# Optimization experiments

Hardware: AMD Instinct MI355X
Metric: run time of the kernel (lower is better)

## Reference

```python
import jax, jax.numpy as jnp
import numpy as np

NUM_HEADS = 2  # embed_dim=8 fixed by n_wires=8 in QLayer

def setup_inputs() -> dict:
    key = jax.random.key(0)
    k1, k2, k3 = jax.random.split(key, 3)
    x = jax.random.normal(k1, (32, 2048, 8), dtype=jnp.float32)
    theta = jax.random.normal(k2, (8,), dtype=jnp.float32)       # trainable RX angles
    W_out = jax.random.normal(k3, (8, 8), dtype=jnp.float32) * 0.35  # out_proj weight (no bias)
    return {"x": x, "theta": theta, "W_out": W_out}

def reference(x, theta, W_out):
    B, S, E = x.shape
    H = NUM_HEADS
    d_k = E // H
    # Quantum layer: RX(x_i) then RX(theta_i) on wire i from |0>, measure PauliZ
    # => <Z_i> = cos(x_i + theta_i). k = q = v = this (three identical calls on x).
    h = jnp.cos(x + theta)                                  # [B, S, E]
    h = h.reshape(B, S, H, d_k).transpose(0, 2, 1, 3)        # [B, H, S, d_k]
    scale = 1.0 / jnp.sqrt(jnp.asarray(d_k, dtype=h.dtype))
    scores = jnp.einsum('bhqd,bhkd->bhqk', h, h) * scale     # [B, H, S, S]
    attn = jax.nn.softmax(scores, axis=-1)                   # dropout: eval-mode identity
    out = jnp.einsum('bhqk,bhkd->bhqd', attn, h)             # [B, H, S, d_k]
    out = out.transpose(0, 2, 1, 3).reshape(B, S, E)         # merge heads
    return out @ W_out.T                                     # nn.Linear(E, E, bias=False)
```

## Files before the change

### kernel.cpp

```cpp
#include <hip/hip_runtime.h>

#define NB 32
#define NS 2048
#define QS 0.72134752044448170367f

typedef _Float16 f16;
typedef _Float16 h2 __attribute__((ext_vector_type(2)));
typedef _Float16 h4 __attribute__((ext_vector_type(4)));
typedef _Float16 h8 __attribute__((ext_vector_type(8)));
typedef float f32x4 __attribute__((ext_vector_type(4)));

__device__ __forceinline__ h2 cvt_pk_f16(float a, float b) {
  return __builtin_bit_cast(h2, __builtin_amdgcn_cvt_pkrtz(a, b));
}
__device__ __forceinline__ f32x4 mfma16(h4 a, h4 b, f32x4 c) {
  return __builtin_amdgcn_mfma_f32_16x16x16f16(a, b, c, 0, 0, 0);
}

#define TR_STRIDE 1032
#define TR_BASE 8192
#define LDS_HALVES (8192 + 10 * 1032)
#define ZIDX (TR_BASE + 9 * TR_STRIDE)

__global__ __launch_bounds__(512, 4) void attn_fused_kernel(
    const float* __restrict__ x, const float* __restrict__ theta,
    const float* __restrict__ Wout, float* __restrict__ outp) {
  __shared__ __align__(16) f16 lds[LDS_HALVES];

  const int b = blockIdx.y;
  const int t = threadIdx.x;
  const int w = t >> 6;
  const int lane = t & 63;
  const int g = lane >> 4;
  const int n = lane & 15;

  float th[8];
#pragma unroll
  for (int e = 0; e < 8; ++e) th[e] = theta[e];

#pragma unroll
  for (int i = 0; i < 2; ++i) {
    const int l = t + 512 * i;
    const float4* xr = (const float4*)(x + ((size_t)b * NS + l) * 8);
    float4 lo = xr[0], hi = xr[1];
    h8 hv;
    hv[0] = (f16)__cosf(lo.x + th[0]);
    hv[1] = (f16)__cosf(lo.y + th[1]);
    hv[2] = (f16)__cosf(lo.z + th[2]);
    hv[3] = (f16)__cosf(lo.w + th[3]);
    hv[4] = (f16)__cosf(hi.x + th[4]);
    hv[5] = (f16)__cosf(hi.y + th[5]);
    hv[6] = (f16)__cosf(hi.z + th[6]);
    hv[7] = (f16)__cosf(hi.w + th[7]);
    ((h8*)lds)[l] = hv;
#pragma unroll
    for (int e = 0; e < 8; ++e) lds[TR_BASE + e * TR_STRIDE + l] = hv[e];
    lds[TR_BASE + 8 * TR_STRIDE + l] = (f16)1.0f;
    lds[ZIDX + l] = (f16)0.0f;
  }

  float4 pf[2][2];
#pragma unroll
  for (int i = 0; i < 2; ++i) {
    const int l = t + 512 * i;
    const float4* xr = (const float4*)(x + ((size_t)b * NS + 1024 + l) * 8);
    pf[i][0] = xr[0];
    pf[i][1] = xr[1];
  }

  h4 Bq0 = {(f16)0.f, (f16)0.f, (f16)0.f, (f16)0.f};
  h4 Bq1 = Bq0;
  if (g == 0) {
    const float4* xq = (const float4*)(
        x + ((size_t)b * NS + blockIdx.x * 128 + w * 16 + n) * 8);
    float4 lo = xq[0], hi = xq[1];
    Bq0[0] = (f16)(__cosf(lo.x + th[0]) * QS);
    Bq0[1] = (f16)(__cosf(lo.y + th[1]) * QS);
    Bq0[2] = (f16)(__cosf(lo.z + th[2]) * QS);
    Bq0[3] = (f16)(__cosf(lo.w + th[3]) * QS);
    Bq1[0] = (f16)(__cosf(hi.x + th[4]) * QS);
    Bq1[1] = (f16)(__cosf(hi.y + th[5]) * QS);
    Bq1[2] = (f16)(__cosf(hi.z + th[6]) * QS);
    Bq1[3] = (f16)(__cosf(hi.w + th[7]) * QS);
  }

  const int sini = (g == 0) ? n * 8 : ZIDX;
  const int sadv = (g == 0) ? 128 : 0;

  const int d0 = (n < 4) ? n : ((n == 4) ? 8 : 9);
  const int d1 = (n < 4) ? (n + 4) : d0;
  const int t0ini = TR_BASE + d0 * TR_STRIDE + 4 * g;
  const int t1ini = TR_BASE + d1 * TR_STRIDE + 4 * g;

  const f32x4 Z = {0.f, 0.f, 0.f, 0.f};
  f32x4 C0 = Z;
  f32x4 C1 = Z;

  __syncthreads();

  for (int chunk = 0; chunk < 2; ++chunk) {
    if (chunk == 1) {
      __syncthreads();
#pragma unroll
      for (int i = 0; i < 2; ++i) {
        const int l = t + 512 * i;
        float4 lo = pf[i][0], hi = pf[i][1];
        h8 hv;
        hv[0] = (f16)__cosf(lo.x + th[0]);
        hv[1] = (f16)__cosf(lo.y + th[1]);
        hv[2] = (f16)__cosf(lo.z + th[2]);
        hv[3] = (f16)__cosf(lo.w + th[3]);
        hv[4] = (f16)__cosf(hi.x + th[4]);
        hv[5] = (f16)__cosf(hi.y + th[5]);
        hv[6] = (f16)__cosf(hi.z + th[6]);
        hv[7] = (f16)__cosf(hi.w + th[7]);
        ((h8*)lds)[l] = hv;
#pragma unroll
        for (int e = 0; e < 8; ++e) lds[TR_BASE + e * TR_STRIDE + l] = hv[e];
      }
      __syncthreads();
    }

    int sa = sini;
    int ta0 = t0ini;
    int ta1 = t1ini;
#pragma unroll 4
    for (int kk = 0; kk < 64; ++kk) {
      h8 kr = *(const h8*)(lds + sa);
      h4 a0 = __builtin_shufflevector(kr, kr, 0, 1, 2, 3);
      h4 a1 = __builtin_shufflevector(kr, kr, 4, 5, 6, 7);
      h4 v0 = *(const h4*)(lds + ta0);
      h4 v1 = *(const h4*)(lds + ta1);

      f32x4 S0 = mfma16(a0, Bq0, Z);
      f32x4 S1 = mfma16(a1, Bq1, Z);

      h4 p0, p1;
      h2 u;
      u = cvt_pk_f16(__builtin_amdgcn_exp2f(S0[0]),
                     __builtin_amdgcn_exp2f(S0[1]));
      p0[0] = u[0];
      p0[1] = u[1];
      u = cvt_pk_f16(__builtin_amdgcn_exp2f(S0[2]),
                     __builtin_amdgcn_exp2f(S0[3]));
      p0[2] = u[0];
      p0[3] = u[1];
      u = cvt_pk_f16(__builtin_amdgcn_exp2f(S1[0]),
                     __builtin_amdgcn_exp2f(S1[1]));
      p1[0] = u[0];
      p1[1] = u[1];
      u = cvt_pk_f16(__builtin_amdgcn_exp2f(S1[2]),
                     __builtin_amdgcn_exp2f(S1[3]));
      p1[2] = u[0];
      p1[3] = u[1];

      C0 = mfma16(v0, p0, C0);
      C1 = mfma16(v1, p1, C1);

      sa += sadv;
      ta0 += 16;
      ta1 += 16;
    }
  }

  const float den0 = __shfl(C0[0], 16 + n, 64);
  const float den1 = __shfl(C1[0], 16 + n, 64);
  if (lane < 16) {
    const float i0 = 1.0f / den0, i1 = 1.0f / den1;
    float m8[8] = {C0[0] * i0, C0[1] * i0, C0[2] * i0, C0[3] * i0,
                   C1[0] * i1, C1[1] * i1, C1[2] * i1, C1[3] * i1};
    float o[8];
#pragma unroll
    for (int e = 0; e < 8; ++e) {
      float s = 0.f;
#pragma unroll
      for (int f = 0; f < 8; ++f) s += m8[f] * Wout[e * 8 + f];
      o[e] = s;
    }
    const int q = blockIdx.x * 128 + w * 16 + n;
    float4* op = (float4*)(outp + ((size_t)b * NS + q) * 8);
    op[0] = make_float4(o[0], o[1], o[2], o[3]);
    op[1] = make_float4(o[4], o[5], o[6], o[7]);
  }
}

extern "C" void kernel_launch(void* const* d_in, const int* in_sizes, int n_in,
                              void* d_out, int out_size, void* d_ws,
                              size_t ws_size, hipStream_t stream) {
  const float* x = (const float*)d_in[0];
  const float* theta = (const float*)d_in[1];
  const float* W = (const float*)d_in[2];
  float* out = (float*)d_out;
  (void)d_ws;
  (void)ws_size;

  attn_fused_kernel<<<dim3(NS / 128, NB), 512, 0, stream>>>(x, theta, W, out);
}
```

Baseline: 89.21 us.

## Split key range across two wave halves per query tile with LDS reduction

```diff
diff --git a/kernel.cpp b/kernel.cpp
--- a/kernel.cpp
+++ b/kernel.cpp
@@ -22,7 +22,7 @@
 #define LDS_HALVES (8192 + 10 * 1032)
 #define ZIDX (TR_BASE + 9 * TR_STRIDE)
 
-__global__ __launch_bounds__(512, 4) void attn_fused_kernel(
+__global__ __launch_bounds__(512, 8) void attn_fused_kernel(
     const float* __restrict__ x, const float* __restrict__ theta,
     const float* __restrict__ Wout, float* __restrict__ outp) {
   __shared__ __align__(16) f16 lds[LDS_HALVES];
@@ -33,6 +33,8 @@
   const int lane = t & 63;
   const int g = lane >> 4;
   const int n = lane & 15;
+  const int qt = w & 3;
+  const int h = w >> 2;
 
   float th[8];
 #pragma unroll
@@ -59,20 +61,11 @@
     lds[ZIDX + l] = (f16)0.0f;
   }
 
-  float4 pf[2][2];
-#pragma unroll
-  for (int i = 0; i < 2; ++i) {
-    const int l = t + 512 * i;
-    const float4* xr = (const float4*)(x + ((size_t)b * NS + 1024 + l) * 8);
-    pf[i][0] = xr[0];
-    pf[i][1] = xr[1];
-  }
-
   h4 Bq0 = {(f16)0.f, (f16)0.f, (f16)0.f, (f16)0.f};
   h4 Bq1 = Bq0;
   if (g == 0) {
     const float4* xq = (const float4*)(
-        x + ((size_t)b * NS + blockIdx.x * 128 + w * 16 + n) * 8);
+        x + ((size_t)b * NS + blockIdx.x * 64 + qt * 16 + n) * 8);
     float4 lo = xq[0], hi = xq[1];
     Bq0[0] = (f16)(__cosf(lo.x + th[0]) * QS);
     Bq0[1] = (f16)(__cosf(lo.y + th[1]) * QS);
@@ -84,13 +77,13 @@
     Bq1[3] = (f16)(__cosf(hi.w + th[7]) * QS);
   }
 
-  const int sini = (g == 0) ? n * 8 : ZIDX;
+  const int sini = (g == 0) ? (h * 512 + n) * 8 : ZIDX;
   const int sadv = (g == 0) ? 128 : 0;
 
   const int d0 = (n < 4) ? n : ((n == 4) ? 8 : 9);
   const int d1 = (n < 4) ? (n + 4) : d0;
-  const int t0ini = TR_BASE + d0 * TR_STRIDE + 4 * g;
-  const int t1ini = TR_BASE + d1 * TR_STRIDE + 4 * g;
+  const int t0ini = TR_BASE + d0 * TR_STRIDE + h * 512 + 4 * g;
+  const int t1ini = TR_BASE + d1 * TR_STRIDE + h * 512 + 4 * g;
 
   const f32x4 Z = {0.f, 0.f, 0.f, 0.f};
   f32x4 C0 = Z;
@@ -104,7 +97,8 @@
 #pragma unroll
       for (int i = 0; i < 2; ++i) {
         const int l = t + 512 * i;
-        float4 lo = pf[i][0], hi = pf[i][1];
+        const float4* xr = (const float4*)(x + ((size_t)b * NS + 1024 + l) * 8);
+        float4 lo = xr[0], hi = xr[1];
         h8 hv;
         hv[0] = (f16)__cosf(lo.x + th[0]);
         hv[1] = (f16)__cosf(lo.y + th[1]);
@@ -125,7 +119,7 @@
     int ta0 = t0ini;
     int ta1 = t1ini;
 #pragma unroll 4
-    for (int kk = 0; kk < 64; ++kk) {
+    for (int kk = 0; kk < 32; ++kk) {
       h8 kr = *(const h8*)(lds + sa);
       h4 a0 = __builtin_shufflevector(kr, kr, 0, 1, 2, 3);
       h4 a1 = __builtin_shufflevector(kr, kr, 4, 5, 6, 7);
@@ -163,24 +157,50 @@
     }
   }
 
-  const float den0 = __shfl(C0[0], 16 + n, 64);
-  const float den1 = __shfl(C1[0], 16 + n, 64);
-  if (lane < 16) {
-    const float i0 = 1.0f / den0, i1 = 1.0f / den1;
-    float m8[8] = {C0[0] * i0, C0[1] * i0, C0[2] * i0, C0[3] * i0,
-                   C1[0] * i1, C1[1] * i1, C1[2] * i1, C1[3] * i1};
-    float o[8];
-#pragma unroll
-    for (int e = 0; e < 8; ++e) {
-      float s = 0.f;
-#pragma unroll
-      for (int f = 0; f < 8; ++f) s += m8[f] * Wout[e * 8 + f];
-      o[e] = s;
+  __syncthreads();
+  float* kvf = (float*)lds;
+  if (h == 1) {
+    float* mb = kvf + ((size_t)(qt * 64 + lane)) * 9;
+    mb[0] = C0[0];
+    mb[1] = C0[1];
+    mb[2] = C0[2];
+    mb[3] = C0[3];
+    mb[4] = C1[0];
+    mb[5] = C1[1];
+    mb[6] = C1[2];
+    mb[7] = C1[3];
+  }
+  __syncthreads();
+  if (h == 0) {
+    const float* mb = kvf + ((size_t)(qt * 64 + lane)) * 9;
+    C0[0] += mb[0];
+    C0[1] += mb[1];
+    C0[2] += mb[2];
+    C0[3] += mb[3];
+    C1[0] += mb[4];
+    C1[1] += mb[5];
+    C1[2] += mb[6];
+    C1[3] += mb[7];
+
+    const float den0 = __shfl(C0[0], 16 + n, 64);
+    const float den1 = __shfl(C1[0], 16 + n, 64);
+    if (lane < 16) {
+      const float i0 = 1.0f / den0, i1 = 1.0f / den1;
+      float m8[8] = {C0[0] * i0, C0[1] * i0, C0[2] * i0, C0[3] * i0,
+                     C1[0] * i1, C1[1] * i1, C1[2] * i1, C1[3] * i1};
+      float o[8];
+#pragma unroll
+      for (int e = 0; e < 8; ++e) {
+        float s = 0.f;
+#pragma unroll
+        for (int f = 0; f < 8; ++f) s += m8[f] * Wout[e * 8 + f];
+        o[e] = s;
+      }
+      const int q = blockIdx.x * 64 + qt * 16 + n;
+      float4* op = (float4*)(outp + ((size_t)b * NS + q) * 8);
+      op[0] = make_float4(o[0], o[1], o[2], o[3]);
+      op[1] = make_float4(o[4], o[5], o[6], o[7]);
     }
-    const int q = blockIdx.x * 128 + w * 16 + n;
-    float4* op = (float4*)(outp + ((size_t)b * NS + q) * 8);
-    op[0] = make_float4(o[0], o[1], o[2], o[3]);
-    op[1] = make_float4(o[4], o[5], o[6], o[7]);
   }
 }
 
@@ -194,5 +214,5 @@
   (void)d_ws;
   (void)ws_size;
 
-  attn_fused_kernel<<<dim3(NS / 128, NB), 512, 0, stream>>>(x, theta, W, out);
-}
+  attn_fused_kernel<<<dim3(NS / 64, NB), 512, 0, stream>>>(x, theta, W, out);
+}
```

After: 91.70 us. 1.03x slower.
